# Kernel optimization log

Measured on AMD Instinct MI355X. Metric: run time of the kernel, lower is better.

## Reference

```python
import jax, jax.numpy as jnp
import numpy as np

N_NODES = 100000
N_EDGES = 1600000
HIDDEN = 128
NUM_RBF = 50
NTYPES = 95
CUTOFF = 5.0


def setup_inputs() -> dict:
    key = jax.random.key(0)
    ks = jax.random.split(key, 10)
    z = jax.random.randint(ks[0], (N_NODES,), 0, NTYPES)
    node_feat = jax.random.normal(ks[1], (N_NODES, HIDDEN), dtype=jnp.float32)
    edge_index = jax.random.randint(ks[2], (2, N_EDGES), 0, N_NODES)
    # distances uniform in [0, 6) so some edges fall beyond the 5.0 cutoff
    edge_weight = jax.random.uniform(ks[3], (N_EDGES,), dtype=jnp.float32) * 6.0
    edge_attr = jax.random.normal(ks[4], (N_EDGES, NUM_RBF), dtype=jnp.float32)
    # learned parameters
    emb = jax.random.normal(ks[5], (NTYPES, HIDDEN), dtype=jnp.float32)
    dp_w = jax.random.normal(ks[6], (HIDDEN, NUM_RBF), dtype=jnp.float32) * (1.0 / np.sqrt(NUM_RBF))
    dp_b = jnp.zeros((HIDDEN,), dtype=jnp.float32)
    comb_w = jax.random.normal(ks[7], (HIDDEN, 2 * HIDDEN), dtype=jnp.float32) * (1.0 / np.sqrt(2 * HIDDEN))
    comb_b = jnp.zeros((HIDDEN,), dtype=jnp.float32)
    return {"z": z, "node_feat": node_feat, "edge_index": edge_index,
            "edge_weight": edge_weight, "edge_attr": edge_attr,
            "emb": emb, "dp_w": dp_w, "dp_b": dp_b,
            "comb_w": comb_w, "comb_b": comb_b}


def cosine_cutoff(r, cutoff):
    c = 0.5 * (jnp.cos(r * (jnp.pi / cutoff)) + 1.0)
    return jnp.where(r < cutoff, c, 0.0)


def reference(z, node_feat, edge_index, edge_weight, edge_attr,
              emb, dp_w, dp_b, comb_w, comb_b):
    # distance filter: [E, H]
    C = cosine_cutoff(edge_weight, CUTOFF)
    W = (edge_attr @ dp_w.T + dp_b) * C[:, None]
    # neighbor-type embedding gathered per edge destination
    x_nb = emb[z]                      # [N, H]
    msg = W * x_nb[edge_index[1]]      # [E, H]
    # scatter-add messages to source nodes
    agg = jnp.zeros_like(node_feat).at[edge_index[0]].add(msg)  # [N, H]
    # combine node features with aggregated neighborhood embedding
    out = jnp.concatenate([node_feat, agg], axis=1) @ comb_w.T + comb_b
    return out
```

## Files before the change

### kernel.cpp

```cpp
#include <hip/hip_runtime.h>

#define HIDDEN 128
#define NRBF 50
#define CUTOFF_F 5.0f
#define PI_OVER_CUTOFF 0.6283185307179586f
#define SLOT_U32 28
#define EPB 512

typedef _Float16 half8_t __attribute__((ext_vector_type(8)));
using f32x4_t  = __attribute__((ext_vector_type(4))) float;
using short8_t = __attribute__((ext_vector_type(8))) short;
typedef __attribute__((ext_vector_type(2))) _Float16 hf2;

static __device__ __forceinline__ unsigned int pkh(float a, float b) {
    return __builtin_bit_cast(unsigned int, __builtin_amdgcn_cvt_pkrtz(a, b));
}
static __device__ __forceinline__ unsigned int pk_bf16(float a, float b) {
    unsigned int ua = __float_as_uint(a), ub = __float_as_uint(b);
    ua = (ua + 0x7FFFu + ((ua >> 16) & 1u)) >> 16;
    ub = (ub + 0x7FFFu + ((ub >> 16) & 1u)) >> 16;
    return ua | (ub << 16);
}


__global__ __launch_bounds__(256) void hist_kernel(
    const int* __restrict__ ei, const float* __restrict__ ew,
    int* __restrict__ cnt, int E)
{
    int e = blockIdx.x * 256 + threadIdx.x;
    if (e >= E) return;
    float r = ew[e];
    if (r < CUTOFF_F) atomicAdd(&cnt[ei[e]], 1);
}

__global__ __launch_bounds__(256) void scan1_kernel(
    const int* __restrict__ cnt, int* __restrict__ rowptr,
    int* __restrict__ bsum, int N)
{
    __shared__ int sh[256];
    int t = threadIdx.x, b = blockIdx.x;
    int base = b * 1024 + t * 4;
    int v[4];
#pragma unroll
    for (int j = 0; j < 4; ++j) v[j] = (base + j < N) ? cnt[base + j] : 0;
    int s = v[0] + v[1] + v[2] + v[3];
    sh[t] = s;
    __syncthreads();
    for (int off = 1; off < 256; off <<= 1) {
        int x = (t >= off) ? sh[t - off] : 0;
        __syncthreads();
        sh[t] += x;
        __syncthreads();
    }
    int run = sh[t] - s;
#pragma unroll
    for (int j = 0; j < 4; ++j) {
        if (base + j < N) rowptr[base + j] = run;
        run += v[j];
    }
    if (t == 255) bsum[b] = sh[255];
}

__global__ __launch_bounds__(256) void scan2_kernel(
    int* __restrict__ bsum, int* __restrict__ rowptr, int nb, int N)
{
    __shared__ int sh[256];
    int t = threadIdx.x;
    int v = (t < nb) ? bsum[t] : 0;
    sh[t] = v;
    __syncthreads();
    for (int off = 1; off < 256; off <<= 1) {
        int x = (t >= off) ? sh[t - off] : 0;
        __syncthreads();
        sh[t] += x;
        __syncthreads();
    }
    if (t < nb) bsum[t] = sh[t] - v;
    if (t == 255) rowptr[N] = sh[255];
}

__global__ __launch_bounds__(256) void scan3_kernel(
    int* __restrict__ rowptr, int* __restrict__ woff,
    const int* __restrict__ bsum, int N)
{
    int t = threadIdx.x, b = blockIdx.x;
    int base = b * 1024 + t * 4;
    int off = bsum[b];
#pragma unroll
    for (int j = 0; j < 4; ++j) {
        int i = base + j;
        if (i < N) {
            int r = rowptr[i] + off;
            rowptr[i] = r;
            woff[i] = r;
        }
    }
}

__global__ __launch_bounds__(256) void pad_kernel(
    const int* __restrict__ rowptr, int N,
    int* __restrict__ desc, unsigned int* __restrict__ slots)
{
    int M = rowptr[N];
    int t = blockIdx.x * 256 + threadIdx.x;
    for (int i = t; i < 512; i += 256 * gridDim.x) desc[M + i] = 0;
    for (int i = t; i < 512 * SLOT_U32; i += 256 * gridDim.x)
        slots[(size_t)M * SLOT_U32 + i] = 0u;
}

__global__ __launch_bounds__(256) void scatter_pack(
    const int* __restrict__ z, const int* __restrict__ ei,
    const float* __restrict__ ew, const float* __restrict__ ea,
    int* __restrict__ woff, int* __restrict__ desc,
    unsigned int* __restrict__ slots, int E)
{
    int e = blockIdx.x * 256 + threadIdx.x;
    if (e >= E) return;
    float r = ew[e];
    if (!(r < CUTOFF_F)) return;
    float C = 0.5f * (cosf(r * PI_OVER_CUTOFF) + 1.0f);
    int src = ei[e];
    int dst = ei[E + e];
    int zt  = z[dst];
    int p = atomicAdd(&woff[src], 1);
    desc[p] = src | (zt << 20);

    unsigned int buf[SLOT_U32];
    const float2* rp = (const float2*)(ea + (size_t)e * NRBF);
#pragma unroll
    for (int q = 0; q < 25; ++q) {
        float2 v = rp[q];
        buf[q] = pkh(C * v.x, C * v.y);
    }
    buf[25] = pkh(C, 0.f);
    buf[26] = 0u; buf[27] = 0u;
    uint4* sp = (uint4*)(slots + (size_t)p * SLOT_U32);
#pragma unroll
    for (int q = 0; q < 7; ++q) sp[q] = ((const uint4*)buf)[q];
}

__global__ __launch_bounds__(256) void scatter_simple(
    const int* __restrict__ z, const int* __restrict__ ei,
    const float* __restrict__ ew, int* __restrict__ woff,
    int* __restrict__ desc, float* __restrict__ cCA, int* __restrict__ eidA,
    int E)
{
    int e = blockIdx.x * 256 + threadIdx.x;
    if (e >= E) return;
    float r = ew[e];
    if (!(r < CUTOFF_F)) return;
    float C = 0.5f * (cosf(r * PI_OVER_CUTOFF) + 1.0f);
    int src = ei[e];
    int dst = ei[E + e];
    int zt  = z[dst];
    int p = atomicAdd(&woff[src], 1);
    desc[p] = src | (zt << 20);
    cCA[p]  = C;
    eidA[p] = e;
}

__global__ __launch_bounds__(256) void gather_mfma(
    const int* __restrict__ rowptr, const int* __restrict__ desc,
    const unsigned int* __restrict__ slots, const float* __restrict__ emb,
    const float* __restrict__ dpw, const float* __restrict__ dpb,
    float* __restrict__ agg, int N)
{
    __shared__ float Wlds[4][16 * 132];
    int M = rowptr[N];

    int nwg = gridDim.x, orig = blockIdx.x;
    int q = nwg >> 3, r8 = nwg & 7, xcd = orig & 7, sub = orig >> 3;
    int lb = (xcd < r8) ? xcd * (q + 1) + sub
                        : r8 * (q + 1) + (xcd - r8) * q + sub;
    int gbase = lb * EPB;
    if (gbase >= M) return;

    int tid  = threadIdx.x;
    int w    = tid >> 6;
    int lane = tid & 63;
    int c    = lane & 15;
    int g    = lane >> 4;

    unsigned int* bstage = (unsigned int*)&Wlds[0][0];
    for (int idx = tid; idx < 128 * 32; idx += 256) {
        int h = idx >> 5, p = idx & 31;
        unsigned int u = 0u;
        if (p < 25) {
            float2 v = *(const float2*)(dpw + h * NRBF + 2 * p);
            u = pkh(v.x, v.y);
        } else if (p == 25) {
            u = pkh(dpb[h], 0.f);
        }
        bstage[h * 36 + p] = u;
    }
    __syncthreads();
    half8_t bfrag[8][2];
#pragma unroll
    for (int nt = 0; nt < 8; ++nt)
#pragma unroll
        for (int ks = 0; ks < 2; ++ks) {
            uint4 bu = *(const uint4*)&bstage[(nt * 16 + c) * 36 + ks * 16 + g * 4];
            bfrag[nt][ks] = __builtin_bit_cast(half8_t, bu);
        }
    __syncthreads();

    float* Ww = &Wlds[w][0];
    int wbeg = gbase + w * 128;
    if (wbeg >= M) return;

    bool runc;
    if (wbeg == 0) runc = true;
    else runc = ((desc[wbeg - 1] & 0xFFFFF) != (desc[wbeg] & 0xFFFFF));

    const int4* dp = (const int4*)(desc + wbeg);

    const uint4* sp0 = (const uint4*)(slots + (size_t)(wbeg + c) * SLOT_U32);
    uint4 a0c = sp0[g];
    uint4 a1c = (g < 3) ? sp0[4 + g] : make_uint4(0u, 0u, 0u, 0u);
    int4 d0 = dp[0], d1 = dp[1], d2 = dp[2], d3 = dp[3];

    int   cur = -1;
    float r0 = 0.f, r1 = 0.f;

    for (int t = 0; t < 8; ++t) {
        int eb = wbeg + t * 16;
        uint4 A0u = a0c, A1u = a1c;
        int s_[16];
        s_[0]=d0.x;  s_[1]=d0.y;  s_[2]=d0.z;  s_[3]=d0.w;
        s_[4]=d1.x;  s_[5]=d1.y;  s_[6]=d1.z;  s_[7]=d1.w;
        s_[8]=d2.x;  s_[9]=d2.y;  s_[10]=d2.z; s_[11]=d2.w;
        s_[12]=d3.x; s_[13]=d3.y; s_[14]=d3.z; s_[15]=d3.w;

        if (t < 7) {
            const uint4* spn = (const uint4*)(slots + (size_t)(eb + 16 + c) * SLOT_U32);
            a0c = spn[g];
            a1c = (g < 3) ? spn[4 + g] : make_uint4(0u, 0u, 0u, 0u);
            d0 = dp[t * 4 + 4]; d1 = dp[t * 4 + 5];
            d2 = dp[t * 4 + 6]; d3 = dp[t * 4 + 7];
        }

        float2 ev[16];
#pragma unroll
        for (int e2 = 0; e2 < 16; ++e2)
            ev[e2] = *(const float2*)(emb + (size_t)((unsigned int)s_[e2] >> 20) * HIDDEN + 2 * lane);

        half8_t A0 = __builtin_bit_cast(half8_t, A0u);
        half8_t A1 = __builtin_bit_cast(half8_t, A1u);
        f32x4_t acc[8];
#pragma unroll
        for (int nt = 0; nt < 8; ++nt) acc[nt] = (f32x4_t){0.f, 0.f, 0.f, 0.f};
#pragma unroll
        for (int nt = 0; nt < 8; ++nt) {
            acc[nt] = __builtin_amdgcn_mfma_f32_16x16x32_f16(A0, bfrag[nt][0], acc[nt], 0, 0, 0);
            acc[nt] = __builtin_amdgcn_mfma_f32_16x16x32_f16(A1, bfrag[nt][1], acc[nt], 0, 0, 0);
        }
#pragma unroll
        for (int nt = 0; nt < 8; ++nt)
#pragma unroll
            for (int r = 0; r < 4; ++r)
                Ww[(g * 4 + r) * 132 + nt * 16 + c] = acc[nt][r];

#pragma unroll
        for (int e2 = 0; e2 < 16; ++e2) {
            int d   = s_[e2];
            int src = d & 0xFFFFF;
            if (src != cur) {
                if (cur >= 0) {
                    float* dst = agg + (size_t)cur * HIDDEN + 2 * lane;
                    if (runc) {
                        *(float2*)dst = make_float2(r0, r1);
                    } else {
                        unsafeAtomicAdd(dst,     r0);
                        unsafeAtomicAdd(dst + 1, r1);
                    }
                    runc = true;
                }
                cur = src; r0 = 0.f; r1 = 0.f;
            }
            float2 wv = *(const float2*)&Ww[e2 * 132 + 2 * lane];
            r0 = fmaf(wv.x, ev[e2].x, r0);
            r1 = fmaf(wv.y, ev[e2].y, r1);
        }
    }
    if (cur >= 0) {
        int nxt = desc[wbeg + 128] & 0xFFFFF;
        float* dst = agg + (size_t)cur * HIDDEN + 2 * lane;
        if (runc && nxt != cur) {
            *(float2*)dst = make_float2(r0, r1);
        } else {
            unsafeAtomicAdd(dst,     r0);
            unsafeAtomicAdd(dst + 1, r1);
        }
    }
}

__global__ __launch_bounds__(256) void gather_stream(
    const int* __restrict__ rowptr, const int* __restrict__ desc,
    const float* __restrict__ cC, const int* __restrict__ eidA,
    const float* __restrict__ ea, const float* __restrict__ emb,
    const float* __restrict__ dpw, const float* __restrict__ dpb,
    float* __restrict__ agg, int N, int nwaves)
{
    __shared__ unsigned int sh_ea[4][4][32];
    int lane  = threadIdx.x & 63;
    int wslot = threadIdx.x >> 6;
    int wid = __builtin_amdgcn_readfirstlane((int)((blockIdx.x * blockDim.x + threadIdx.x) >> 6));

    hf2 whA[25], whB[25];
    {
        const float* wr0 = dpw + (size_t)(2 * lane) * NRBF;
        const float* wr1 = wr0 + NRBF;
#pragma unroll
        for (int q = 0; q < 25; ++q) {
            float2 x = *(const float2*)(wr0 + 2 * q);
            float2 y = *(const float2*)(wr1 + 2 * q);
            whA[q] = __builtin_bit_cast(hf2, pkh(x.x, x.y));
            whB[q] = __builtin_bit_cast(hf2, pkh(y.x, y.y));
        }
    }
    float2 db = *(const float2*)(dpb + 2 * lane);

    int M  = rowptr[N];
    int CH = (M + nwaves - 1) / nwaves;
    int c0 = min(wid * CH, M);
    int c1 = min(c0 + CH, M);

    int   cur = -1, run_start = c0;
    float a0 = 0.f, a1 = 0.f;

    for (int i = c0; i < c1; i += 4) {
        int sv[4]; float cf[4]; int ed[4]; float2 ev[4]; float2 eaf[4];
#pragma unroll
        for (int j = 0; j < 4; ++j)
            if (i + j < c1) { sv[j] = desc[i + j]; cf[j] = cC[i + j]; ed[j] = eidA[i + j]; }
#pragma unroll
        for (int j = 0; j < 4; ++j)
            if (i + j < c1) ev[j] = *(const float2*)(emb + (size_t)((unsigned int)sv[j] >> 20) * HIDDEN + 2 * lane);
#pragma unroll
        for (int j = 0; j < 4; ++j)
            if (i + j < c1 && lane < 25) eaf[j] = *(const float2*)(ea + (size_t)ed[j] * NRBF + 2 * lane);
#pragma unroll
        for (int j = 0; j < 4; ++j)
            if (i + j < c1 && lane < 28) {
                unsigned int u = 0u;
                if (lane < 25) u = pkh(eaf[j].x, eaf[j].y);
                sh_ea[wslot][j][lane] = u;
            }
#pragma unroll
        for (int j = 0; j < 4; ++j) {
            if (i + j >= c1) break;
            int src = sv[j] & 0xFFFFF;
            if (src != cur) {
                if (cur >= 0) {
                    int rp0 = rowptr[cur], rp1 = rowptr[cur + 1];
                    float* dst = agg + (size_t)cur * HIDDEN + 2 * lane;
                    if (run_start == rp0 && (i + j) == rp1) {
                        *(float2*)dst = make_float2(a0, a1);
                    } else {
                        unsafeAtomicAdd(dst, a0);
                        unsafeAtomicAdd(dst + 1, a1);
                    }
                }
                cur = src; run_start = i + j; a0 = 0.f; a1 = 0.f;
            }
            float s0 = 0.f, s1 = 0.f;
#pragma unroll
            for (int qq = 0; qq < 6; ++qq) {
                uint4 u = *(const uint4*)&sh_ea[wslot][j][qq * 4];
#pragma unroll
                for (int t = 0; t < 4; ++t) {
                    unsigned int ww = (t == 0) ? u.x : (t == 1) ? u.y : (t == 2) ? u.z : u.w;
                    hf2 e2 = __builtin_bit_cast(hf2, ww);
                    s0 = fmaf((float)e2[0], (float)whA[qq*4+t][0], fmaf((float)e2[1], (float)whA[qq*4+t][1], s0));
                    s1 = fmaf((float)e2[0], (float)whB[qq*4+t][0], fmaf((float)e2[1], (float)whB[qq*4+t][1], s1));
                }
            }
            {
                hf2 e2 = __builtin_bit_cast(hf2, sh_ea[wslot][j][24]);
                s0 = fmaf((float)e2[0], (float)whA[24][0], fmaf((float)e2[1], (float)whA[24][1], s0));
                s1 = fmaf((float)e2[0], (float)whB[24][0], fmaf((float)e2[1], (float)whB[24][1], s1));
            }
            float W0 = (s0 + db.x) * cf[j];
            float W1 = (s1 + db.y) * cf[j];
            a0 = fmaf(W0, ev[j].x, a0);
            a1 = fmaf(W1, ev[j].y, a1);
        }
    }
    if (cur >= 0) {
        int rp0 = rowptr[cur], rp1 = rowptr[cur + 1];
        float* dst = agg + (size_t)cur * HIDDEN + 2 * lane;
        if (run_start == rp0 && c1 == rp1) {
            *(float2*)dst = make_float2(a0, a1);
        } else {
            unsafeAtomicAdd(dst, a0);
            unsafeAtomicAdd(dst + 1, a1);
        }
    }
}

__global__ __launch_bounds__(256) void edge_kernel(
    const int* __restrict__ z, const int* __restrict__ ei,
    const float* __restrict__ ew, const float* __restrict__ ea,
    const float* __restrict__ emb, const float* __restrict__ dpw,
    const float* __restrict__ dpb, float* __restrict__ agg, int E)
{
    int e = blockIdx.x * 256 + threadIdx.x;
    if (e >= E) return;
    float r = ew[e];
    if (!(r < CUTOFF_F)) return;
    float C = 0.5f * (cosf(r * PI_OVER_CUTOFF) + 1.0f);
    int src = ei[e];
    int dst = ei[E + e];
    int zt  = z[dst];
    float av[NRBF];
#pragma unroll
    for (int k = 0; k < NRBF; ++k) av[k] = ea[(size_t)e * NRBF + k];
    const float* er = emb + (size_t)zt * HIDDEN;
    float*       ar = agg + (size_t)src * HIDDEN;
#pragma unroll 2
    for (int h = 0; h < HIDDEN; ++h) {
        const float* wrow = dpw + h * NRBF;
        float s0 = 0.f, s1 = 0.f;
#pragma unroll
        for (int k = 0; k < NRBF; k += 2) {
            s0 = fmaf(av[k],     wrow[k],     s0);
            s1 = fmaf(av[k + 1], wrow[k + 1], s1);
        }
        float w2 = (dpb[h] + s0 + s1) * C;
        unsafeAtomicAdd(&ar[h], w2 * er[h]);
    }
}

__global__ __launch_bounds__(256) void combine_mfma(
    const float* __restrict__ nf, const float* __restrict__ cw,
    const float* __restrict__ cbias, float* out, int N)
{
    __shared__ unsigned int As_u[64 * 20];
    __shared__ unsigned int Bs_u[128 * 20];
    int tid  = threadIdx.x;
    int w    = tid >> 6;
    int lane = tid & 63;
    int c    = lane & 15;
    int g    = lane >> 4;
    int row0 = blockIdx.x * 64;

    f32x4_t acc[8];
#pragma unroll
    for (int q = 0; q < 8; ++q) acc[q] = (f32x4_t){0.f, 0.f, 0.f, 0.f};

    for (int ks = 0; ks < 8; ++ks) {
        const float* src = (ks < 4) ? nf : out;
        int kb = (ks & 3) * 32;
        {
            int r = tid >> 2, kq = tid & 3;
            int row = row0 + r;
            float4 v0 = make_float4(0.f, 0.f, 0.f, 0.f), v1 = v0;
            if (row < N) {
                const float4* p = (const float4*)(src + (size_t)row * HIDDEN + kb + kq * 8);
                v0 = p[0]; v1 = p[1];
            }
            *(uint4*)&As_u[r * 20 + kq * 4] =
                make_uint4(pk_bf16(v0.x, v0.y), pk_bf16(v0.z, v0.w),
                           pk_bf16(v1.x, v1.y), pk_bf16(v1.z, v1.w));
        }
        {
            int j = tid >> 1, hf = tid & 1;
            const float4* p = (const float4*)(cw + (size_t)j * 256 + ks * 32 + hf * 16);
            float4 b0 = p[0], b1 = p[1], b2 = p[2], b3 = p[3];
            *(uint4*)&Bs_u[j * 20 + hf * 8] =
                make_uint4(pk_bf16(b0.x, b0.y), pk_bf16(b0.z, b0.w),
                           pk_bf16(b1.x, b1.y), pk_bf16(b1.z, b1.w));
            *(uint4*)&Bs_u[j * 20 + hf * 8 + 4] =
                make_uint4(pk_bf16(b2.x, b2.y), pk_bf16(b2.z, b2.w),
                           pk_bf16(b3.x, b3.y), pk_bf16(b3.z, b3.w));
        }
        __syncthreads();
        uint4 au = *(const uint4*)&As_u[(w * 16 + c) * 20 + g * 4];
        short8_t af = __builtin_bit_cast(short8_t, au);
#pragma unroll
        for (int cbk = 0; cbk < 8; ++cbk) {
            uint4 bu = *(const uint4*)&Bs_u[(cbk * 16 + c) * 20 + g * 4];
            short8_t bf = __builtin_bit_cast(short8_t, bu);
            acc[cbk] = __builtin_amdgcn_mfma_f32_16x16x32_bf16(af, bf, acc[cbk], 0, 0, 0);
        }
        __syncthreads();
    }
#pragma unroll
    for (int cbk = 0; cbk < 8; ++cbk) {
        float bias = cbias[cbk * 16 + c];
#pragma unroll
        for (int r = 0; r < 4; ++r) {
            int row = row0 + w * 16 + g * 4 + r;
            if (row < N) out[(size_t)row * HIDDEN + cbk * 16 + c] = acc[cbk][r] + bias;
        }
    }
}


extern "C" void kernel_launch(void* const* d_in, const int* in_sizes, int n_in,
                              void* d_out, int out_size, void* d_ws, size_t ws_size,
                              hipStream_t stream)
{
    const int*   z   = (const int*)  d_in[0];
    const float* nf  = (const float*)d_in[1];
    const int*   ei  = (const int*)  d_in[2];
    const float* ew  = (const float*)d_in[3];
    const float* ea  = (const float*)d_in[4];
    const float* emb = (const float*)d_in[5];
    const float* dpw = (const float*)d_in[6];
    const float* dpb = (const float*)d_in[7];
    const float* cw  = (const float*)d_in[8];
    const float* cb  = (const float*)d_in[9];
    float* out = (float*)d_out;

    int N = in_sizes[0];
    int E = in_sizes[3];

    size_t hdr  = ((size_t)2 * N + 1 + 1024 + 3) & ~(size_t)3;
    size_t Epad = (size_t)E + 512;
    size_t need1 = (hdr + Epad + Epad * SLOT_U32 + 8) * 4;
    size_t need2 = (hdr + (size_t)3 * E) * 4;

    (void)hipMemsetAsync(out, 0, (size_t)N * HIDDEN * sizeof(float), stream);

    int nb1 = (N + 1023) / 1024;

    if (ws_size >= need1) {
        int* rowptr = (int*)d_ws;
        int* woff   = rowptr + (N + 1);
        int* bsum   = woff + N;
        int* desc   = (int*)d_ws + hdr;
        unsigned int* slots = (unsigned int*)(desc + Epad);
        slots = (unsigned int*)(((size_t)slots + 15) & ~(size_t)15);

        (void)hipMemsetAsync(woff, 0, (size_t)N * 4, stream);
        hist_kernel<<<(E + 255) / 256, 256, 0, stream>>>(ei, ew, woff, E);
        scan1_kernel<<<nb1, 256, 0, stream>>>(woff, rowptr, bsum, N);
        scan2_kernel<<<1, 256, 0, stream>>>(bsum, rowptr, nb1, N);
        scan3_kernel<<<nb1, 256, 0, stream>>>(rowptr, woff, bsum, N);
        scatter_pack<<<(E + 255) / 256, 256, 0, stream>>>(z, ei, ew, ea, woff,
                                                          desc, slots, E);
        pad_kernel<<<8, 256, 0, stream>>>(rowptr, N, desc, slots);
        int nblk = (E + EPB - 1) / EPB;
        gather_mfma<<<nblk, 256, 0, stream>>>(rowptr, desc, slots, emb,
                                              dpw, dpb, out, N);
    } else if (ws_size >= need2) {
        int* rowptr = (int*)d_ws;
        int* woff   = rowptr + (N + 1);
        int* bsum   = woff + N;
        int* desc   = (int*)d_ws + hdr;
        float* cCA  = (float*)(desc + E);
        int* eidA   = (int*)(cCA + E);

        (void)hipMemsetAsync(woff, 0, (size_t)N * 4, stream);
        hist_kernel<<<(E + 255) / 256, 256, 0, stream>>>(ei, ew, woff, E);
        scan1_kernel<<<nb1, 256, 0, stream>>>(woff, rowptr, bsum, N);
        scan2_kernel<<<1, 256, 0, stream>>>(bsum, rowptr, nb1, N);
        scan3_kernel<<<nb1, 256, 0, stream>>>(rowptr, woff, bsum, N);
        scatter_simple<<<(E + 255) / 256, 256, 0, stream>>>(z, ei, ew, woff,
                                                            desc, cCA, eidA, E);
        const int blocks = 2048;
        gather_stream<<<blocks, 256, 0, stream>>>(rowptr, desc, cCA, eidA,
                                                  ea, emb, dpw, dpb, out, N,
                                                  blocks * 4);
    } else {
        edge_kernel<<<(E + 255) / 256, 256, 0, stream>>>(z, ei, ew, ea, emb,
                                                         dpw, dpb, out, E);
    }

    combine_mfma<<<(N + 63) / 64, 256, 0, stream>>>(nf, cw, cb, out, N);
}
```

Baseline: 452.1 us.

## Read MFMA B fragments from LDS and pack embeddings and filter weights to fp16

The gather kernel no longer keeps the 16 B-operand fragments in registers; it reads them from a padded LDS array on each tile, which frees many VGPRs and can raise occupancy. The embedding table is packed to fp16 pairs by a new small kernel, and the per-edge filter values are staged in LDS as fp16 pairs, so gather and LDS traffic shrink by half. Descriptors are made wave-uniform with readfirstlane, and output columns are remapped to lane and lane+64. The cost is more LDS reads per tile and extra fp16 rounding of the embeddings and filter weights.

```diff
diff --git a/kernel.cpp b/kernel.cpp
--- a/kernel.cpp
+++ b/kernel.cpp
@@ -6,6 +6,8 @@
 #define PI_OVER_CUTOFF 0.6283185307179586f
 #define SLOT_U32 28
 #define EPB 512
+#define B_PITCH 35
+#define W_PITCH 66
 
 typedef _Float16 half8_t __attribute__((ext_vector_type(8)));
 using f32x4_t  = __attribute__((ext_vector_type(4))) float;
@@ -14,6 +16,12 @@
 
 static __device__ __forceinline__ unsigned int pkh(float a, float b) {
     return __builtin_bit_cast(unsigned int, __builtin_amdgcn_cvt_pkrtz(a, b));
+}
+static __device__ __forceinline__ float cvlo(unsigned int u) {
+    return (float)__builtin_bit_cast(hf2, u)[0];
+}
+static __device__ __forceinline__ float cvhi(unsigned int u) {
+    return (float)__builtin_bit_cast(hf2, u)[1];
 }
 static __device__ __forceinline__ unsigned int pk_bf16(float a, float b) {
     unsigned int ua = __float_as_uint(a), ub = __float_as_uint(b);
@@ -106,6 +114,15 @@
     for (int i = t; i < 512; i += 256 * gridDim.x) desc[M + i] = 0;
     for (int i = t; i < 512 * SLOT_U32; i += 256 * gridDim.x)
         slots[(size_t)M * SLOT_U32 + i] = 0u;
+}
+
+__global__ __launch_bounds__(256) void pack_emb(
+    const float* __restrict__ emb, unsigned int* __restrict__ embp, int NT)
+{
+    int i = blockIdx.x * 256 + threadIdx.x;
+    if (i >= NT * 64) return;
+    int t = i >> 6, j = i & 63;
+    embp[i] = pkh(emb[t * HIDDEN + j], emb[t * HIDDEN + j + 64]);
 }
 
 __global__ __launch_bounds__(256) void scatter_pack(
@@ -161,11 +178,12 @@
 
 __global__ __launch_bounds__(256) void gather_mfma(
     const int* __restrict__ rowptr, const int* __restrict__ desc,
-    const unsigned int* __restrict__ slots, const float* __restrict__ emb,
+    const unsigned int* __restrict__ slots, const unsigned int* __restrict__ embp,
     const float* __restrict__ dpw, const float* __restrict__ dpb,
     float* __restrict__ agg, int N)
 {
-    __shared__ float Wlds[4][16 * 132];
+    __shared__ unsigned int Blds[128 * B_PITCH];
+    __shared__ unsigned int Wlds[4][16 * W_PITCH];
     int M = rowptr[N];
 
     int nwg = gridDim.x, orig = blockIdx.x;
@@ -181,7 +199,6 @@
     int c    = lane & 15;
     int g    = lane >> 4;
 
-    unsigned int* bstage = (unsigned int*)&Wlds[0][0];
     for (int idx = tid; idx < 128 * 32; idx += 256) {
         int h = idx >> 5, p = idx & 31;
         unsigned int u = 0u;
@@ -191,20 +208,11 @@
         } else if (p == 25) {
             u = pkh(dpb[h], 0.f);
         }
-        bstage[h * 36 + p] = u;
+        Blds[h * B_PITCH + p] = u;
     }
     __syncthreads();
-    half8_t bfrag[8][2];
-#pragma unroll
-    for (int nt = 0; nt < 8; ++nt)
-#pragma unroll
-        for (int ks = 0; ks < 2; ++ks) {
-            uint4 bu = *(const uint4*)&bstage[(nt * 16 + c) * 36 + ks * 16 + g * 4];
-            bfrag[nt][ks] = __builtin_bit_cast(half8_t, bu);
-        }
-    __syncthreads();
-
-    float* Ww = &Wlds[w][0];
+
+    unsigned int* Ww = Wlds[w];
     int wbeg = gbase + w * 128;
     if (wbeg >= M) return;
 
@@ -226,10 +234,14 @@
         int eb = wbeg + t * 16;
         uint4 A0u = a0c, A1u = a1c;
         int s_[16];
-        s_[0]=d0.x;  s_[1]=d0.y;  s_[2]=d0.z;  s_[3]=d0.w;
-        s_[4]=d1.x;  s_[5]=d1.y;  s_[6]=d1.z;  s_[7]=d1.w;
-        s_[8]=d2.x;  s_[9]=d2.y;  s_[10]=d2.z; s_[11]=d2.w;
-        s_[12]=d3.x; s_[13]=d3.y; s_[14]=d3.z; s_[15]=d3.w;
+        s_[0]=__builtin_amdgcn_readfirstlane(d0.x);  s_[1]=__builtin_amdgcn_readfirstlane(d0.y);
+        s_[2]=__builtin_amdgcn_readfirstlane(d0.z);  s_[3]=__builtin_amdgcn_readfirstlane(d0.w);
+        s_[4]=__builtin_amdgcn_readfirstlane(d1.x);  s_[5]=__builtin_amdgcn_readfirstlane(d1.y);
+        s_[6]=__builtin_amdgcn_readfirstlane(d1.z);  s_[7]=__builtin_amdgcn_readfirstlane(d1.w);
+        s_[8]=__builtin_amdgcn_readfirstlane(d2.x);  s_[9]=__builtin_amdgcn_readfirstlane(d2.y);
+        s_[10]=__builtin_amdgcn_readfirstlane(d2.z); s_[11]=__builtin_amdgcn_readfirstlane(d2.w);
+        s_[12]=__builtin_amdgcn_readfirstlane(d3.x); s_[13]=__builtin_amdgcn_readfirstlane(d3.y);
+        s_[14]=__builtin_amdgcn_readfirstlane(d3.z); s_[15]=__builtin_amdgcn_readfirstlane(d3.w);
 
         if (t < 7) {
             const uint4* spn = (const uint4*)(slots + (size_t)(eb + 16 + c) * SLOT_U32);
@@ -239,57 +251,65 @@
             d2 = dp[t * 4 + 6]; d3 = dp[t * 4 + 7];
         }
 
-        float2 ev[16];
+        unsigned int evp[16];
 #pragma unroll
         for (int e2 = 0; e2 < 16; ++e2)
-            ev[e2] = *(const float2*)(emb + (size_t)((unsigned int)s_[e2] >> 20) * HIDDEN + 2 * lane);
+            evp[e2] = embp[(((unsigned int)s_[e2]) >> 20) * 64 + lane];
 
         half8_t A0 = __builtin_bit_cast(half8_t, A0u);
         half8_t A1 = __builtin_bit_cast(half8_t, A1u);
         f32x4_t acc[8];
 #pragma unroll
-        for (int nt = 0; nt < 8; ++nt) acc[nt] = (f32x4_t){0.f, 0.f, 0.f, 0.f};
-#pragma unroll
         for (int nt = 0; nt < 8; ++nt) {
-            acc[nt] = __builtin_amdgcn_mfma_f32_16x16x32_f16(A0, bfrag[nt][0], acc[nt], 0, 0, 0);
-            acc[nt] = __builtin_amdgcn_mfma_f32_16x16x32_f16(A1, bfrag[nt][1], acc[nt], 0, 0, 0);
-        }
-#pragma unroll
-        for (int nt = 0; nt < 8; ++nt)
+            uint4 b0 = *(const uint4*)&Blds[(nt * 16 + c) * B_PITCH + g * 4];
+            uint4 b1 = *(const uint4*)&Blds[(nt * 16 + c) * B_PITCH + 16 + g * 4];
+            f32x4_t a = (f32x4_t){0.f, 0.f, 0.f, 0.f};
+            a = __builtin_amdgcn_mfma_f32_16x16x32_f16(A0, __builtin_bit_cast(half8_t, b0), a, 0, 0, 0);
+            a = __builtin_amdgcn_mfma_f32_16x16x32_f16(A1, __builtin_bit_cast(half8_t, b1), a, 0, 0, 0);
+            acc[nt] = a;
+        }
+
+#pragma unroll
+        for (int m = 0; m < 4; ++m)
 #pragma unroll
             for (int r = 0; r < 4; ++r)
-                Ww[(g * 4 + r) * 132 + nt * 16 + c] = acc[nt][r];
+                Ww[(g * 4 + r) * W_PITCH + m * 16 + c] = pkh(acc[m][r], acc[m + 4][r]);
+
+        unsigned int wv[16];
+#pragma unroll
+        for (int e2 = 0; e2 < 16; ++e2)
+            wv[e2] = Ww[e2 * W_PITCH + lane];
 
 #pragma unroll
         for (int e2 = 0; e2 < 16; ++e2) {
-            int d   = s_[e2];
-            int src = d & 0xFFFFF;
+            int src = s_[e2] & 0xFFFFF;
             if (src != cur) {
                 if (cur >= 0) {
-                    float* dst = agg + (size_t)cur * HIDDEN + 2 * lane;
+                    float* dst = agg + (size_t)cur * HIDDEN + lane;
                     if (runc) {
-                        *(float2*)dst = make_float2(r0, r1);
+                        dst[0]  = r0;
+                        dst[64] = r1;
                     } else {
-                        unsafeAtomicAdd(dst,     r0);
-                        unsafeAtomicAdd(dst + 1, r1);
+                        unsafeAtomicAdd(dst,      r0);
+                        unsafeAtomicAdd(dst + 64, r1);
                     }
                     runc = true;
                 }
                 cur = src; r0 = 0.f; r1 = 0.f;
             }
-            float2 wv = *(const float2*)&Ww[e2 * 132 + 2 * lane];
-            r0 = fmaf(wv.x, ev[e2].x, r0);
-            r1 = fmaf(wv.y, ev[e2].y, r1);
+            r0 = fmaf(cvlo(wv[e2]), cvlo(evp[e2]), r0);
+            r1 = fmaf(cvhi(wv[e2]), cvhi(evp[e2]), r1);
         }
     }
     if (cur >= 0) {
         int nxt = desc[wbeg + 128] & 0xFFFFF;
-        float* dst = agg + (size_t)cur * HIDDEN + 2 * lane;
+        float* dst = agg + (size_t)cur * HIDDEN + lane;
         if (runc && nxt != cur) {
-            *(float2*)dst = make_float2(r0, r1);
+            dst[0]  = r0;
+            dst[64] = r1;
         } else {
-            unsafeAtomicAdd(dst,     r0);
-            unsafeAtomicAdd(dst + 1, r1);
+            unsafeAtomicAdd(dst,      r0);
+            unsafeAtomicAdd(dst + 64, r1);
         }
     }
 }
@@ -515,10 +535,11 @@
 
     int N = in_sizes[0];
     int E = in_sizes[3];
+    int NT = in_sizes[5] / HIDDEN;
 
     size_t hdr  = ((size_t)2 * N + 1 + 1024 + 3) & ~(size_t)3;
     size_t Epad = (size_t)E + 512;
-    size_t need1 = (hdr + Epad + Epad * SLOT_U32 + 8) * 4;
+    size_t need1 = (hdr + Epad + Epad * SLOT_U32 + (size_t)NT * 64 + 16) * 4;
     size_t need2 = (hdr + (size_t)3 * E) * 4;
 
     (void)hipMemsetAsync(out, 0, (size_t)N * HIDDEN * sizeof(float), stream);
@@ -532,17 +553,19 @@
         int* desc   = (int*)d_ws + hdr;
         unsigned int* slots = (unsigned int*)(desc + Epad);
         slots = (unsigned int*)(((size_t)slots + 15) & ~(size_t)15);
+        unsigned int* embp = slots + Epad * SLOT_U32;
 
         (void)hipMemsetAsync(woff, 0, (size_t)N * 4, stream);
         hist_kernel<<<(E + 255) / 256, 256, 0, stream>>>(ei, ew, woff, E);
         scan1_kernel<<<nb1, 256, 0, stream>>>(woff, rowptr, bsum, N);
         scan2_kernel<<<1, 256, 0, stream>>>(bsum, rowptr, nb1, N);
         scan3_kernel<<<nb1, 256, 0, stream>>>(rowptr, woff, bsum, N);
+        pack_emb<<<(NT * 64 + 255) / 256, 256, 0, stream>>>(emb, embp, NT);
         scatter_pack<<<(E + 255) / 256, 256, 0, stream>>>(z, ei, ew, ea, woff,
                                                           desc, slots, E);
         pad_kernel<<<8, 256, 0, stream>>>(rowptr, N, desc, slots);
         int nblk = (E + EPB - 1) / EPB;
-        gather_mfma<<<nblk, 256, 0, stream>>>(rowptr, desc, slots, emb,
+        gather_mfma<<<nblk, 256, 0, stream>>>(rowptr, desc, slots, embp,
                                               dpw, dpb, out, N);
     } else if (ws_size >= need2) {
         int* rowptr = (int*)d_ws;
```

Measured after the change: 393.1 us. 13.1% less time.
